# Kernel tuning notes

Measured on AMD Instinct MI355X. Metric: run time of the kernel, lower is better.

Reference implementation:

```python
import jax, jax.numpy as jnp
import numpy as np

INNER_LR = 0.01        # inner-loop fast-weight learning rate
ADAPTER_SCALE = 1.0    # adapter_scale from __init__
INIT_STD = 0.001       # init_std for phi_0 fast-weight initialization
VOCAB = 32000


def setup_inputs() -> dict:
    key = jax.random.key(0)
    k1, k2, k3, k4, k5 = jax.random.split(key, 5)
    B, S, H, R, V = 2, 2048, 1024, 16, VOCAB
    hidden_states = jax.random.normal(k1, (B, S, H), dtype=jnp.float32)
    input_ids = jax.random.randint(k2, (B, S), 0, V)
    # phi_0 learned fast-weight initialization (init_std-scaled, per TTTMetaAdapter)
    fast_a = jax.random.normal(k3, (H, R), dtype=jnp.float32) * INIT_STD
    fast_b = jax.random.normal(k4, (R, H), dtype=jnp.float32) * INIT_STD
    lm_head = jax.random.normal(k5, (H, V), dtype=jnp.float32) * 0.02
    return {"hidden_states": hidden_states, "input_ids": input_ids,
            "fast_a": fast_a, "fast_b": fast_b, "lm_head": lm_head}


def _next_token_loss(logits, input_ids):
    # ttt_next_token_loss_from_logits: CE(logits[:, :-1], input_ids[:, 1:])
    logp = jax.nn.log_softmax(logits[:, :-1, :], axis=-1)       # [B, S-1, V]
    tgt = input_ids[:, 1:]                                       # [B, S-1]
    nll = -jnp.take_along_axis(logp, tgt[..., None], axis=-1)[..., 0]
    return nll.mean()


def _apply(hidden_states, a, b):
    # TTTState.apply: h + (h @ fast_a @ fast_b) * scale
    return hidden_states + ((hidden_states @ a) @ b) * ADAPTER_SCALE


def reference(hidden_states, input_ids, fast_a, fast_b, lm_head):
    # Inner objective: next-token CE of adapted hidden states through lm_head.
    def inner_loss(a, b):
        adapted = _apply(hidden_states, a, b)                    # [B, S, H]
        logits = adapted @ lm_head                               # [B, S, V]
        return _next_token_loss(logits, input_ids)

    loss, (ga, gb) = jax.value_and_grad(inner_loss, argnums=(0, 1))(fast_a, fast_b)
    grad_norm = jnp.sqrt(jnp.sum(ga * ga) + jnp.sum(gb * gb))
    # One differentiable TTT inner gradient step on the fast weights.
    new_a = fast_a - INNER_LR * ga
    new_b = fast_b - INNER_LR * gb
    out = _apply(hidden_states, new_a, new_b)                    # adapted output
    return out, new_a, new_b, loss, grad_norm
```

## Files before the change

### kernel.cpp

```cpp
#include <hip/hip_runtime.h>
#include <hip/hip_bf16.h>


#define ROWS 4096
#define Hdim 1024
#define Rdim 16
#define Vdim 32000
#define NVALID 4094.0f
#define LRATE 0.01f
#define RB 32
#define VT 512
#define LAS 1032

typedef __attribute__((ext_vector_type(8))) short bf16x8;
typedef __attribute__((ext_vector_type(4))) float f32x4;

static __device__ __forceinline__ float bf2f(short u) {
  union { float f; unsigned int i; } w; w.i = ((unsigned int)(unsigned short)u) << 16; return w.f;
}
static __device__ __forceinline__ short f2bf(float f) {
  union { float f; unsigned int i; } w; w.f = f;
  unsigned int lsb = (w.i >> 16) & 1u;
  w.i += 0x7fffu + lsb;
  return (short)(w.i >> 16);
}
static __device__ __forceinline__ f32x4 mfma16(bf16x8 a, bf16x8 b, f32x4 c) {
  return __builtin_amdgcn_mfma_f32_16x16x32_bf16(a, b, c, 0, 0, 0);
}
static __device__ __forceinline__ f32x4 mfma8(long a, long b, f32x4 c) {
  return __builtin_amdgcn_mfma_f32_16x16x32_fp8_fp8(a, b, c, 0, 0, 0);
}
static __device__ __forceinline__ int pk4fp8(float f0, float f1, float f2, float f3) {
  int v = __builtin_amdgcn_cvt_pk_fp8_f32(f0, f1, 0, false);
  v = __builtin_amdgcn_cvt_pk_fp8_f32(f2, f3, v, true);
  return v;
}

#define OFF_BP2   ((size_t)0)
#define OFF_BP1   ((size_t)65536000)
#define OFF_ADP   ((size_t)98304000)
#define OFF_ADP8  ((size_t)106692608)
#define OFF_DA    ((size_t)110886912)
#define OFF_U     ((size_t)127664128)
#define OFF_DU    ((size_t)127926272)
#define OFF_Z     ((size_t)128188416)
#define OFF_GA    ((size_t)128221184)
#define OFF_GB    ((size_t)128286720)
#define OFF_LOSS  ((size_t)128352256)

#define OUT_A    ((size_t)4194304)
#define OUT_B    ((size_t)4210688)
#define OUT_LOSS ((size_t)4227072)
#define OUT_GN   ((size_t)4227073)

__global__ void k_pack(const float* __restrict__ in, char* __restrict__ Bp1,
                       short* __restrict__ Bp2) {
  __shared__ float tile[32][260];
  int v0 = blockIdx.x * 256, k0 = blockIdx.y * 32;
  int tid = threadIdx.x;
#pragma unroll
  for (int r = 0; r < 32; ++r)
    tile[r][tid] = in[(size_t)(k0 + r) * Vdim + v0 + tid];
  __syncthreads();
  int lane = tid & 63, l15 = lane & 15, q = (lane >> 4) & 3, g = tid >> 6;
#pragma unroll
  for (int it = 0; it < 4; ++it) {
    int vbl = it * 4 + g;
    float f[8];
#pragma unroll
    for (int j = 0; j < 8; ++j) f[j] = tile[q * 8 + j][vbl * 16 + l15];
    int2 w2;
    w2.x = pk4fp8(f[0], f[1], f[2], f[3]);
    w2.y = pk4fp8(f[4], f[5], f[6], f[7]);
    *(int2*)(Bp1 + ((size_t)(v0 / 16 + vbl) * 32 + k0 / 32) * 512 + lane * 8) = w2;
  }
#pragma unroll
  for (int it = 0; it < 4; ++it) {
    int idx = it * 4 + g;
    int hbl = idx >> 3, vkbl = idx & 7;
    bf16x8 frag;
#pragma unroll
    for (int j = 0; j < 8; ++j) frag[j] = f2bf(tile[hbl * 16 + l15][vkbl * 32 + q * 8 + j]);
    *(bf16x8*)(Bp2 + ((size_t)(k0 / 16 + hbl) * 1000 + v0 / 32 + vkbl) * 512 + lane * 8) = frag;
  }
}

__global__ void k_prep_ua(const float* __restrict__ hs, const float* __restrict__ fa,
                          const float* __restrict__ fb, float* __restrict__ u,
                          short* __restrict__ adp, char* __restrict__ adp8) {
  __shared__ float wred[4][16];
  __shared__ float ubc[16];
  int row = blockIdx.x, tid = threadIdx.x, lane = tid & 63, w = tid >> 6;
  const float* hrow = hs + (size_t)row * Hdim;
  float4 hv = *(const float4*)(hrow + tid * 4);
  float ur[16];
  const float* fap = fa + (size_t)tid * 4 * Rdim;
#pragma unroll
  for (int r = 0; r < 16; ++r)
    ur[r] = hv.x * fap[r] + hv.y * fap[16 + r] + hv.z * fap[32 + r] + hv.w * fap[48 + r];
#pragma unroll
  for (int r = 0; r < 16; ++r)
#pragma unroll
    for (int off = 32; off; off >>= 1) ur[r] += __shfl_xor(ur[r], off);
  if (lane == 0) {
#pragma unroll
    for (int r = 0; r < 16; ++r) wred[w][r] = ur[r];
  }
  __syncthreads();
  if (tid < 16) {
    float s = wred[0][tid] + wred[1][tid] + wred[2][tid] + wred[3][tid];
    ubc[tid] = s;
    u[row * Rdim + tid] = s;
  }
  __syncthreads();
  float a0 = hv.x, a1 = hv.y, a2 = hv.z, a3 = hv.w;
#pragma unroll
  for (int r = 0; r < 16; ++r) {
    float uv = ubc[r];
    float4 bv = *(const float4*)(fb + r * Hdim + tid * 4);
    a0 += uv * bv.x; a1 += uv * bv.y; a2 += uv * bv.z; a3 += uv * bv.w;
  }
  short4 o; o.x = f2bf(a0); o.y = f2bf(a1); o.z = f2bf(a2); o.w = f2bf(a3);
  *(short4*)(adp + (size_t)row * Hdim + tid * 4) = o;
  *(int*)(adp8 + (size_t)row * Hdim + tid * 4) = pk4fp8(a0, a1, a2, a3);
}

__launch_bounds__(1024, 4)
__global__ void k_fused(const char* __restrict__ adp8, const char* __restrict__ Bp1,
                        const short* __restrict__ Bp2, short* __restrict__ dApart,
                        float* __restrict__ zpart) {
  __shared__ __align__(16) char lA[RB * LAS];
  __shared__ __align__(16) short lP[2][RB * VT];
  __shared__ float zred[RB * 16];
  int tid = threadIdx.x, lane = tid & 63, w = tid >> 6;
  int q = lane >> 4, l15 = lane & 15;
  int L = blockIdx.x;
  int sp = (L >> 2) & 1;
  int rg = (L & 3) | ((L >> 3) << 2);
  int row0 = rg * RB;
  int v0beg = sp ? 15872 : 0;
  int v0end = sp ? 32000 : 15872;
  int nt = sp ? 32 : 31;

#pragma unroll
  for (int i = 0; i < 4; ++i) {
    int idx = tid + i * 1024;
    int r = idx >> 7, kk8 = (idx & 127) * 8;
    *(int2*)(lA + r * LAS + kk8) = *(const int2*)(adp8 + (size_t)(row0 + r) * Hdim + kk8);
  }
  if (tid < RB * 16) zred[tid] = 0.f;

  f32x4 acc[2][4];
#pragma unroll
  for (int rf = 0; rf < 2; ++rf)
#pragma unroll
    for (int cf = 0; cf < 4; ++cf)
#pragma unroll
      for (int i = 0; i < 4; ++i) acc[rf][cf][i] = 0.f;

  __syncthreads();

  for (int t = 0; t < nt; ++t) {
    int v0 = v0beg + t * VT;
    int rem = v0end - v0; if (rem > VT) rem = VT;
    char* lPc = (char*)lP[t & 1];
    f32x4 lacc[2][2];
#pragma unroll
    for (int rf = 0; rf < 2; ++rf)
#pragma unroll
      for (int cf = 0; cf < 2; ++cf)
#pragma unroll
        for (int i = 0; i < 4; ++i) lacc[rf][cf][i] = 0.f;
#pragma unroll 8
    for (int ks = 0; ks < 32; ++ks) {
      int kk = ks * 32 + q * 8;
      long af[2], bfr[2];
      af[0] = *(const long*)(lA + l15 * LAS + kk);
      af[1] = *(const long*)(lA + (16 + l15) * LAS + kk);
#pragma unroll
      for (int cf = 0; cf < 2; ++cf) {
        int vb = v0 / 16 + w * 2 + cf;
        if (vb > 1999) vb = 1999;
        bfr[cf] = *(const long*)(Bp1 + ((size_t)vb * 32 + ks) * 512 + lane * 8);
      }
#pragma unroll
      for (int rf = 0; rf < 2; ++rf)
#pragma unroll
        for (int cf = 0; cf < 2; ++cf)
          lacc[rf][cf] = mfma8(af[rf], bfr[cf], lacc[rf][cf]);
    }
#pragma unroll
    for (int rf = 0; rf < 2; ++rf)
#pragma unroll
      for (int i = 0; i < 4; ++i) {
        int r = rf * 16 + q * 4 + i;
        float z = 0.f;
#pragma unroll
        for (int cf = 0; cf < 2; ++cf) {
          int c0 = w * 32 + cf * 16;
          float pv = (c0 < rem) ? __expf(lacc[rf][cf][i]) : 0.f;
          z += pv;
          int c = c0 + l15;
          *(short*)(lPc + r * 1024 + ((c * 2) ^ ((r & 7) << 4))) = f2bf(pv);
        }
#pragma unroll
        for (int off = 1; off < 16; off <<= 1) z += __shfl_xor(z, off);
        if (l15 == 0) zred[r * 16 + w] += z;
      }
    __syncthreads();
#pragma unroll 4
    for (int ks = 0; ks < 16; ++ks) {
      int kb = ks * 32 + q * 8;
      int vkb = v0 / 32 + ks;
      if (vkb > 999) vkb = 999;
      bf16x8 pa[2], bg[4];
#pragma unroll
      for (int rf = 0; rf < 2; ++rf) {
        int r = rf * 16 + l15;
        pa[rf] = *(const bf16x8*)(lPc + r * 1024 + ((kb * 2) ^ ((r & 7) << 4)));
      }
#pragma unroll
      for (int cf = 0; cf < 4; ++cf)
        bg[cf] = *(const bf16x8*)(Bp2 + ((size_t)(w * 4 + cf) * 1000 + vkb) * 512 + lane * 8);
#pragma unroll
      for (int rf = 0; rf < 2; ++rf)
#pragma unroll
        for (int cf = 0; cf < 4; ++cf)
          acc[rf][cf] = mfma16(pa[rf], bg[cf], acc[rf][cf]);
    }
  }
  __syncthreads();
  if (tid < RB) {
    float z = 0.f;
#pragma unroll
    for (int g = 0; g < 16; ++g) z += zred[tid * 16 + g];
    zpart[sp * ROWS + row0 + tid] = z;
  }
#pragma unroll
  for (int rf = 0; rf < 2; ++rf)
#pragma unroll
    for (int cf = 0; cf < 4; ++cf)
#pragma unroll
      for (int i = 0; i < 4; ++i) {
        int r = rf * 16 + q * 4 + i;
        int h = w * 64 + cf * 16 + l15;
        dApart[((size_t)(row0 + r) * 2 + sp) * Hdim + h] = f2bf(acc[rf][cf][i]);
      }
}

__global__ void k_post_du(const short* __restrict__ adp, const short* __restrict__ Bp2,
                          const float* __restrict__ fb, const int* __restrict__ ids,
                          const float* __restrict__ zpart, char* __restrict__ dAx,
                          float* __restrict__ du, float* __restrict__ loss_acc) {
  __shared__ float red[256];
  __shared__ float wredu[4][16];
  int row = blockIdx.x, tid = threadIdx.x, lane = tid & 63, w = tid >> 6;
  int b = row >> 11, s = row & 2047;
  bool valid = s < 2047;
  float Z = zpart[row] + zpart[ROWS + row];
  float sc = 1.f / (Z * NVALID);
  int tgt = valid ? ids[b * 2048 + s + 1] : 0;
  const short* prow = (const short*)(dAx + (size_t)row * 4096);
  short4 p0 = *(const short4*)(prow + tid * 4);
  short4 p1 = *(const short4*)(prow + 1024 + tid * 4);
  short4 a4 = *(const short4*)(adp + (size_t)row * Hdim + tid * 4);
  int tq = (tgt >> 3) & 3, tj = tgt & 7, tvkb = tgt >> 5;
  float lcv[4], d[4];
#pragma unroll
  for (int c = 0; c < 4; ++c) {
    int h = tid * 4 + c;
    short lcs = Bp2[((size_t)(h >> 4) * 1000 + tvkb) * 512 +
                    (size_t)(((h & 15) + 16 * tq) * 8 + tj)];
    lcv[c] = bf2f(lcs);
  }
  float q0[4] = {bf2f(p0.x), bf2f(p0.y), bf2f(p0.z), bf2f(p0.w)};
  float q1[4] = {bf2f(p1.x), bf2f(p1.y), bf2f(p1.z), bf2f(p1.w)};
  float avv[4] = {bf2f(a4.x), bf2f(a4.y), bf2f(a4.z), bf2f(a4.w)};
#pragma unroll
  for (int c = 0; c < 4; ++c)
    d[c] = valid ? ((q0[c] + q1[c]) * sc - lcv[c] * (1.f / NVALID)) : 0.f;
  __syncthreads();
  float* drow = (float*)(dAx + (size_t)row * 4096);
  float dot = 0.f;
#pragma unroll
  for (int c = 0; c < 4; ++c) {
    drow[tid * 4 + c] = d[c];
    dot += avv[c] * lcv[c];
  }
  float pdu[16];
#pragma unroll
  for (int r = 0; r < 16; ++r) {
    float4 bv = *(const float4*)(fb + r * Hdim + tid * 4);
    pdu[r] = d[0] * bv.x + d[1] * bv.y + d[2] * bv.z + d[3] * bv.w;
  }
#pragma unroll
  for (int r = 0; r < 16; ++r)
#pragma unroll
    for (int off = 32; off; off >>= 1) pdu[r] += __shfl_xor(pdu[r], off);
  if (lane == 0) {
#pragma unroll
    for (int r = 0; r < 16; ++r) wredu[w][r] = pdu[r];
  }
  red[tid] = dot;
  __syncthreads();
  if (tid < 16)
    du[row * Rdim + tid] = wredu[0][tid] + wredu[1][tid] + wredu[2][tid] + wredu[3][tid];
  if (!valid) return;
  for (int o = 128; o; o >>= 1) {
    if (tid < o) red[tid] += red[tid + o];
    __syncthreads();
  }
  if (tid == 0) atomicAdd(loss_acc, (logf(Z) - red[0]) / NVALID);
}

__global__ void k_ga_gb(const float* __restrict__ hs, const float* __restrict__ dA,
                        const float* __restrict__ u, const float* __restrict__ du,
                        float* __restrict__ ga, float* __restrict__ gb) {
  __shared__ float lu[512 * 16], ldu[512 * 16];
  int tid = threadIdx.x;
  int h = blockIdx.x * 256 + tid;
  int r0 = blockIdx.y * 512;
#pragma unroll
  for (int i = 0; i < 32; ++i) {
    int idx = tid + i * 256;
    lu[idx] = u[(size_t)r0 * Rdim + idx];
    ldu[idx] = du[(size_t)r0 * Rdim + idx];
  }
  __syncthreads();
  float aga[16], agb[16];
#pragma unroll
  for (int r = 0; r < 16; ++r) { aga[r] = 0.f; agb[r] = 0.f; }
  for (int rl = 0; rl < 512; ++rl) {
    int row = r0 + rl;
    float hv = hs[(size_t)row * Hdim + h];
    float dv = dA[(size_t)row * Hdim + h];
#pragma unroll
    for (int r = 0; r < 16; ++r) {
      aga[r] += hv * ldu[rl * 16 + r];
      agb[r] += lu[rl * 16 + r] * dv;
    }
  }
#pragma unroll
  for (int r = 0; r < 16; ++r) {
    atomicAdd(&ga[h * Rdim + r], aga[r]);
    atomicAdd(&gb[r * Hdim + h], agb[r]);
  }
}

__global__ void k_finalize(const float* __restrict__ fa, const float* __restrict__ fb,
                           const float* __restrict__ ga, const float* __restrict__ gb,
                           const float* __restrict__ loss_acc, float* __restrict__ out) {
  __shared__ float red[512];
  int tid = threadIdx.x;
  float s = 0.f;
  for (int i = tid; i < 32768; i += 512) {
    float g = ga[i];
    s += g * g;
  }
  red[tid] = s; __syncthreads();
  for (int o = 256; o; o >>= 1) {
    if (tid < o) red[tid] += red[tid + o];
    __syncthreads();
  }
  float gn = sqrtf(red[0]);
  for (int i = tid; i < 16384; i += 512) {
    out[OUT_A + i] = fa[i] - LRATE * ga[i];
    out[OUT_B + i] = fb[i] - LRATE * gb[i];
  }
  if (tid == 0) { out[OUT_LOSS] = loss_acc[0]; out[OUT_GN] = gn; }
}

__global__ void k_tail_uo(const float* __restrict__ hs, const float* __restrict__ outAB,
                          float* __restrict__ out) {
  __shared__ float wred[4][16];
  __shared__ float ubc[16];
  int row = blockIdx.x, tid = threadIdx.x, lane = tid & 63, w = tid >> 6;
  const float* na = outAB;
  const float* nb = outAB + 16384;
  const float* hrow = hs + (size_t)row * Hdim;
  float4 hv = *(const float4*)(hrow + tid * 4);
  float ur[16];
  const float* nap = na + (size_t)tid * 4 * Rdim;
#pragma unroll
  for (int r = 0; r < 16; ++r)
    ur[r] = hv.x * nap[r] + hv.y * nap[16 + r] + hv.z * nap[32 + r] + hv.w * nap[48 + r];
#pragma unroll
  for (int r = 0; r < 16; ++r)
#pragma unroll
    for (int off = 32; off; off >>= 1) ur[r] += __shfl_xor(ur[r], off);
  if (lane == 0) {
#pragma unroll
    for (int r = 0; r < 16; ++r) wred[w][r] = ur[r];
  }
  __syncthreads();
  if (tid < 16) ubc[tid] = wred[0][tid] + wred[1][tid] + wred[2][tid] + wred[3][tid];
  __syncthreads();
  float a0 = hv.x, a1 = hv.y, a2 = hv.z, a3 = hv.w;
#pragma unroll
  for (int r = 0; r < 16; ++r) {
    float uv = ubc[r];
    float4 bv = *(const float4*)(nb + r * Hdim + tid * 4);
    a0 += uv * bv.x; a1 += uv * bv.y; a2 += uv * bv.z; a3 += uv * bv.w;
  }
  float4 o; o.x = a0; o.y = a1; o.z = a2; o.w = a3;
  *(float4*)(out + (size_t)row * Hdim + tid * 4) = o;
}

extern "C" void kernel_launch(void* const* d_in, const int* in_sizes, int n_in,
                              void* d_out, int out_size, void* d_ws, size_t ws_size,
                              hipStream_t stream) {
  (void)in_sizes; (void)n_in; (void)out_size; (void)ws_size;
  const float* hs   = (const float*)d_in[0];
  const int*   ids  = (const int*)d_in[1];
  const float* fa   = (const float*)d_in[2];
  const float* fb   = (const float*)d_in[3];
  const float* lmhf = (const float*)d_in[4];
  float* out = (float*)d_out;
  char* ws = (char*)d_ws;

  short* Bp2    = (short*)(ws + OFF_BP2);
  char*  Bp1    = ws + OFF_BP1;
  short* adp    = (short*)(ws + OFF_ADP);
  char*  adp8   = ws + OFF_ADP8;
  char*  dAx    = ws + OFF_DA;
  float* u      = (float*)(ws + OFF_U);
  float* du     = (float*)(ws + OFF_DU);
  float* zpart  = (float*)(ws + OFF_Z);
  float* ga     = (float*)(ws + OFF_GA);
  float* gb     = (float*)(ws + OFF_GB);
  float* loss_acc = (float*)(ws + OFF_LOSS);

  hipMemsetAsync(ws + OFF_GA, 0, 65536 * 2 + 4, stream);

  k_pack<<<dim3(125, 32), 256, 0, stream>>>(lmhf, Bp1, Bp2);
  k_prep_ua<<<4096, 256, 0, stream>>>(hs, fa, fb, u, adp, adp8);
  k_fused<<<256, 1024, 0, stream>>>(adp8, Bp1, Bp2, (short*)dAx, zpart);
  k_post_du<<<4096, 256, 0, stream>>>(adp, Bp2, fb, ids, zpart, dAx, du, loss_acc);
  k_ga_gb<<<dim3(4, 8), 256, 0, stream>>>(hs, (float*)dAx, u, du, ga, gb);
  k_finalize<<<1, 512, 0, stream>>>(fa, fb, ga, gb, loss_acc, out);
  k_tail_uo<<<4096, 256, 0, stream>>>(hs, out + OUT_A, out);
}
```

Before: 1.017 ms.

## Switch backward P@lm_head^T GEMM to FP8 MFMA with transposed bf16 gather table

Both the softmax probability tile and the packed lm_head^T operand of the second GEMM in the fused kernel are now stored as FP8 instead of bf16. The GEMM therefore uses the fp8 MFMA, which halves LDS and global traffic for that operand and has higher throughput. A separate bf16 transposed lm_head copy is added so the target-column gather in k_post_du becomes a contiguous vector load. Per-tile shuffle reductions of Z are replaced by register accumulation reduced once at the end. The cost is lower precision in dA, plus extra pack-time writes for the transposed table.

```diff
diff --git a/kernel.cpp b/kernel.cpp
--- a/kernel.cpp
+++ b/kernel.cpp
@@ -24,9 +24,6 @@
   w.i += 0x7fffu + lsb;
   return (short)(w.i >> 16);
 }
-static __device__ __forceinline__ f32x4 mfma16(bf16x8 a, bf16x8 b, f32x4 c) {
-  return __builtin_amdgcn_mfma_f32_16x16x32_bf16(a, b, c, 0, 0, 0);
-}
 static __device__ __forceinline__ f32x4 mfma8(long a, long b, f32x4 c) {
   return __builtin_amdgcn_mfma_f32_16x16x32_fp8_fp8(a, b, c, 0, 0, 0);
 }
@@ -35,18 +32,22 @@
   v = __builtin_amdgcn_cvt_pk_fp8_f32(f2, f3, v, true);
   return v;
 }
+static __device__ __forceinline__ char fp8_1(float f) {
+  return (char)(__builtin_amdgcn_cvt_pk_fp8_f32(f, 0.f, 0, false) & 0xff);
+}
 
 #define OFF_BP2   ((size_t)0)
-#define OFF_BP1   ((size_t)65536000)
-#define OFF_ADP   ((size_t)98304000)
-#define OFF_ADP8  ((size_t)106692608)
-#define OFF_DA    ((size_t)110886912)
-#define OFF_U     ((size_t)127664128)
-#define OFF_DU    ((size_t)127926272)
-#define OFF_Z     ((size_t)128188416)
-#define OFF_GA    ((size_t)128221184)
-#define OFF_GB    ((size_t)128286720)
-#define OFF_LOSS  ((size_t)128352256)
+#define OFF_BP1   ((size_t)32768000)
+#define OFF_LMHT  ((size_t)65536000)
+#define OFF_ADP   ((size_t)131072000)
+#define OFF_ADP8  ((size_t)139460608)
+#define OFF_DA    ((size_t)143654912)
+#define OFF_U     ((size_t)160432128)
+#define OFF_DU    ((size_t)160694272)
+#define OFF_Z     ((size_t)160956416)
+#define OFF_GA    ((size_t)160989184)
+#define OFF_GB    ((size_t)161054720)
+#define OFF_LOSS  ((size_t)161120256)
 
 #define OUT_A    ((size_t)4194304)
 #define OUT_B    ((size_t)4210688)
@@ -54,7 +55,7 @@
 #define OUT_GN   ((size_t)4227073)
 
 __global__ void k_pack(const float* __restrict__ in, char* __restrict__ Bp1,
-                       short* __restrict__ Bp2) {
+                       char* __restrict__ Bp2, short* __restrict__ lmhT) {
   __shared__ float tile[32][260];
   int v0 = blockIdx.x * 256, k0 = blockIdx.y * 32;
   int tid = threadIdx.x;
@@ -78,10 +79,20 @@
   for (int it = 0; it < 4; ++it) {
     int idx = it * 4 + g;
     int hbl = idx >> 3, vkbl = idx & 7;
-    bf16x8 frag;
-#pragma unroll
-    for (int j = 0; j < 8; ++j) frag[j] = f2bf(tile[hbl * 16 + l15][vkbl * 32 + q * 8 + j]);
-    *(bf16x8*)(Bp2 + ((size_t)(k0 / 16 + hbl) * 1000 + v0 / 32 + vkbl) * 512 + lane * 8) = frag;
+    float f[8];
+#pragma unroll
+    for (int j = 0; j < 8; ++j) f[j] = tile[hbl * 16 + l15][vkbl * 32 + q * 8 + j];
+    int2 w2;
+    w2.x = pk4fp8(f[0], f[1], f[2], f[3]);
+    w2.y = pk4fp8(f[4], f[5], f[6], f[7]);
+    *(int2*)(Bp2 + ((size_t)(k0 / 16 + hbl) * 1000 + v0 / 32 + vkbl) * 512 + lane * 8) = w2;
+  }
+#pragma unroll
+  for (int jj = 0; jj < 4; ++jj) {
+    bf16x8 fr;
+#pragma unroll
+    for (int j = 0; j < 8; ++j) fr[j] = f2bf(tile[jj * 8 + j][tid]);
+    *(bf16x8*)(lmhT + (size_t)(v0 + tid) * 1024 + k0 + jj * 8) = fr;
   }
 }
 
@@ -127,10 +138,10 @@
 
 __launch_bounds__(1024, 4)
 __global__ void k_fused(const char* __restrict__ adp8, const char* __restrict__ Bp1,
-                        const short* __restrict__ Bp2, short* __restrict__ dApart,
+                        const char* __restrict__ Bp2, short* __restrict__ dApart,
                         float* __restrict__ zpart) {
   __shared__ __align__(16) char lA[RB * LAS];
-  __shared__ __align__(16) short lP[2][RB * VT];
+  __shared__ __align__(16) char lP[2][RB * 512];
   __shared__ float zred[RB * 16];
   int tid = threadIdx.x, lane = tid & 63, w = tid >> 6;
   int q = lane >> 4, l15 = lane & 15;
@@ -148,9 +159,11 @@
     int r = idx >> 7, kk8 = (idx & 127) * 8;
     *(int2*)(lA + r * LAS + kk8) = *(const int2*)(adp8 + (size_t)(row0 + r) * Hdim + kk8);
   }
-  if (tid < RB * 16) zred[tid] = 0.f;
-
+
+  float zacc[8];
   f32x4 acc[2][4];
+#pragma unroll
+  for (int j = 0; j < 8; ++j) zacc[j] = 0.f;
 #pragma unroll
   for (int rf = 0; rf < 2; ++rf)
 #pragma unroll
@@ -194,18 +207,14 @@
 #pragma unroll
       for (int i = 0; i < 4; ++i) {
         int r = rf * 16 + q * 4 + i;
-        float z = 0.f;
 #pragma unroll
         for (int cf = 0; cf < 2; ++cf) {
           int c0 = w * 32 + cf * 16;
           float pv = (c0 < rem) ? __expf(lacc[rf][cf][i]) : 0.f;
-          z += pv;
+          zacc[rf * 4 + i] += pv;
           int c = c0 + l15;
-          *(short*)(lPc + r * 1024 + ((c * 2) ^ ((r & 7) << 4))) = f2bf(pv);
+          lPc[r * 512 + (((c & ~7) ^ ((r & 7) << 3)) | (c & 7))] = fp8_1(pv);
         }
-#pragma unroll
-        for (int off = 1; off < 16; off <<= 1) z += __shfl_xor(z, off);
-        if (l15 == 0) zred[r * 16 + w] += z;
       }
     __syncthreads();
 #pragma unroll 4
@@ -213,22 +222,31 @@
       int kb = ks * 32 + q * 8;
       int vkb = v0 / 32 + ks;
       if (vkb > 999) vkb = 999;
-      bf16x8 pa[2], bg[4];
+      long pa[2], bg[4];
 #pragma unroll
       for (int rf = 0; rf < 2; ++rf) {
         int r = rf * 16 + l15;
-        pa[rf] = *(const bf16x8*)(lPc + r * 1024 + ((kb * 2) ^ ((r & 7) << 4)));
+        pa[rf] = *(const long*)(lPc + r * 512 + (kb ^ ((r & 7) << 3)));
       }
 #pragma unroll
       for (int cf = 0; cf < 4; ++cf)
-        bg[cf] = *(const bf16x8*)(Bp2 + ((size_t)(w * 4 + cf) * 1000 + vkb) * 512 + lane * 8);
+        bg[cf] = *(const long*)(Bp2 + ((size_t)(w * 4 + cf) * 1000 + vkb) * 512 + lane * 8);
 #pragma unroll
       for (int rf = 0; rf < 2; ++rf)
 #pragma unroll
         for (int cf = 0; cf < 4; ++cf)
-          acc[rf][cf] = mfma16(pa[rf], bg[cf], acc[rf][cf]);
+          acc[rf][cf] = mfma8(pa[rf], bg[cf], acc[rf][cf]);
     }
   }
+#pragma unroll
+  for (int rf = 0; rf < 2; ++rf)
+#pragma unroll
+    for (int i = 0; i < 4; ++i) {
+      float z = zacc[rf * 4 + i];
+#pragma unroll
+      for (int off = 1; off < 16; off <<= 1) z += __shfl_xor(z, off);
+      if (l15 == 0) zred[(rf * 16 + q * 4 + i) * 16 + w] = z;
+    }
   __syncthreads();
   if (tid < RB) {
     float z = 0.f;
@@ -248,7 +266,7 @@
       }
 }
 
-__global__ void k_post_du(const short* __restrict__ adp, const short* __restrict__ Bp2,
+__global__ void k_post_du(const short* __restrict__ adp, const short* __restrict__ lmhT,
                           const float* __restrict__ fb, const int* __restrict__ ids,
                           const float* __restrict__ zpart, char* __restrict__ dAx,
                           float* __restrict__ du, float* __restrict__ loss_acc) {
@@ -264,18 +282,12 @@
   short4 p0 = *(const short4*)(prow + tid * 4);
   short4 p1 = *(const short4*)(prow + 1024 + tid * 4);
   short4 a4 = *(const short4*)(adp + (size_t)row * Hdim + tid * 4);
-  int tq = (tgt >> 3) & 3, tj = tgt & 7, tvkb = tgt >> 5;
-  float lcv[4], d[4];
-#pragma unroll
-  for (int c = 0; c < 4; ++c) {
-    int h = tid * 4 + c;
-    short lcs = Bp2[((size_t)(h >> 4) * 1000 + tvkb) * 512 +
-                    (size_t)(((h & 15) + 16 * tq) * 8 + tj)];
-    lcv[c] = bf2f(lcs);
-  }
+  short4 lc4 = *(const short4*)(lmhT + (size_t)tgt * 1024 + tid * 4);
+  float lcv[4] = {bf2f(lc4.x), bf2f(lc4.y), bf2f(lc4.z), bf2f(lc4.w)};
   float q0[4] = {bf2f(p0.x), bf2f(p0.y), bf2f(p0.z), bf2f(p0.w)};
   float q1[4] = {bf2f(p1.x), bf2f(p1.y), bf2f(p1.z), bf2f(p1.w)};
   float avv[4] = {bf2f(a4.x), bf2f(a4.y), bf2f(a4.z), bf2f(a4.w)};
+  float d[4];
 #pragma unroll
   for (int c = 0; c < 4; ++c)
     d[c] = valid ? ((q0[c] + q1[c]) * sc - lcv[c] * (1.f / NVALID)) : 0.f;
@@ -418,8 +430,9 @@
   float* out = (float*)d_out;
   char* ws = (char*)d_ws;
 
-  short* Bp2    = (short*)(ws + OFF_BP2);
+  char*  Bp2    = ws + OFF_BP2;
   char*  Bp1    = ws + OFF_BP1;
+  short* lmhT   = (short*)(ws + OFF_LMHT);
   short* adp    = (short*)(ws + OFF_ADP);
   char*  adp8   = ws + OFF_ADP8;
   char*  dAx    = ws + OFF_DA;
@@ -432,10 +445,10 @@
 
   hipMemsetAsync(ws + OFF_GA, 0, 65536 * 2 + 4, stream);
 
-  k_pack<<<dim3(125, 32), 256, 0, stream>>>(lmhf, Bp1, Bp2);
+  k_pack<<<dim3(125, 32), 256, 0, stream>>>(lmhf, Bp1, Bp2, lmhT);
   k_prep_ua<<<4096, 256, 0, stream>>>(hs, fa, fb, u, adp, adp8);
   k_fused<<<256, 1024, 0, stream>>>(adp8, Bp1, Bp2, (short*)dAx, zpart);
-  k_post_du<<<4096, 256, 0, stream>>>(adp, Bp2, fb, ids, zpart, dAx, du, loss_acc);
+  k_post_du<<<4096, 256, 0, stream>>>(adp, lmhT, fb, ids, zpart, dAx, du, loss_acc);
   k_ga_gb<<<dim3(4, 8), 256, 0, stream>>>(hs, (float*)dAx, u, du, ga, gb);
   k_finalize<<<1, 512, 0, stream>>>(fa, fb, ga, gb, loss_acc, out);
   k_tail_uo<<<4096, 256, 0, stream>>>(hs, out + OUT_A, out);
```

Measured after the change: 1.117 ms. 1.1x slower.
